# Optimization experiments

Hardware: AMD Instinct MI355X
Metric: run time of the kernel (lower is better)

Reference implementation:

```python
import jax, jax.numpy as jnp
import numpy as np

B, T, C, H = 2, 2048, 1024, 16
HD = C // H          # head_dim = 64
RD = HD // 2         # rotary half-dim = 32


def _rope_tables(T, rd, base=10000.0):
    inv_freq = 1.0 / (base ** (np.arange(rd, dtype=np.float32) / rd))
    t = np.arange(T, dtype=np.float32)
    ang = np.outer(t, inv_freq)  # [T, rd]
    cos = np.cos(ang)[None, :, None, :]  # [1,T,1,rd]
    sin = np.sin(ang)[None, :, None, :]
    return jnp.asarray(cos), jnp.asarray(sin)


def setup_inputs() -> dict:
    key = jax.random.key(0)
    k1, k2, k3 = jax.random.split(key, 3)
    cos, sin = _rope_tables(T, RD)
    return {
        "x": jax.random.normal(k1, (B, T, C), dtype=jnp.float32),
        "cos": cos,
        "sin": sin,
        "W_qkv": jax.random.normal(k2, (C, C), dtype=jnp.float32) / np.sqrt(C),
        "W_proj": jax.random.normal(k3, (C, C), dtype=jnp.float32) / np.sqrt(C),
        "window_left": 512,
    }


def _apply_rotary(x, cos, sin):
    # x: [B,T,H,HD]
    x1, x2 = x[..., :RD], x[..., RD:]
    y1 = x1 * cos + x2 * sin
    y2 = -x1 * sin + x2 * cos
    return jnp.concatenate([y1, y2], axis=-1)


def _rms_norm(x):
    eps = jnp.finfo(x.dtype).eps
    ms = jnp.mean(jnp.square(x), axis=-1, keepdims=True)
    return x * jax.lax.rsqrt(ms + eps)


def reference(x, cos, sin, W_qkv, W_proj, window_left):
    Bx, Tx, Cx = x.shape
    scale = HD ** -0.5
    # tied QKV projection (single matmul)
    w = jnp.einsum("btc,cd->btd", x, W_qkv).reshape(Bx, Tx, H, HD)
    w = _apply_rotary(w, cos, sin)
    w = _rms_norm(w)                      # [B,T,H,HD]
    wq = jnp.transpose(w, (0, 2, 1, 3))    # [B,H,T,HD]
    dots = jnp.einsum("bhqd,bhkd->bhqk", wq, wq) * scale  # [B,H,T,T]
    # causal + sliding-window mask: allow 0 <= (q - k) <= window_left
    i = jnp.arange(Tx)[:, None]
    j = jnp.arange(Tx)[None, :]
    dist = i - j
    allowed = (dist >= 0) & ((window_left <= 0) | (dist <= window_left))
    dots = jnp.where(allowed, dots, -jnp.inf)
    attn = jax.nn.softmax(dots, axis=-1)
    out = jnp.einsum("bhqk,bhkd->bhqd", attn, wq)
    out = jnp.transpose(out, (0, 2, 1, 3)).reshape(Bx, Tx, Cx)
    return jnp.einsum("btc,cd->btd", out, W_proj)
```

## Files before the change

kernel.cpp:

```cpp
#include <hip/hip_runtime.h>
#include <hip/hip_bf16.h>

typedef __bf16 bf16_t;
typedef __bf16 bf16x4 __attribute__((ext_vector_type(4)));
typedef __bf16 bf16x8 __attribute__((ext_vector_type(8)));
typedef float f32x4 __attribute__((ext_vector_type(4)));

#define B_ 2
#define T_ 2048
#define C_ 1024
#define H_ 16
#define HD_ 64
#define RD_ 32
#define M_ (B_ * T_)

__global__ __launch_bounds__(256) void k_prep(const float* __restrict__ x,
                                              bf16_t* __restrict__ xb,
                                              const float* __restrict__ Wq,
                                              bf16_t* __restrict__ wqt,
                                              const float* __restrict__ Wp,
                                              bf16_t* __restrict__ wpt) {
    const int bid = blockIdx.x;
    if (bid < 4096) {
        int i = bid * 256 + threadIdx.x;
        float4 v = reinterpret_cast<const float4*>(x)[i];
        bf16x4 o;
        o[0] = (bf16_t)v.x; o[1] = (bf16_t)v.y; o[2] = (bf16_t)v.z; o[3] = (bf16_t)v.w;
        reinterpret_cast<bf16x4*>(xb)[i] = o;
    } else {
        __shared__ float tile[32][33];
        int b2 = bid - 4096;
        const float* W = (b2 < 1024) ? Wq : Wp;
        bf16_t* Wt = (b2 < 1024) ? wqt : wpt;
        b2 &= 1023;
        const int n0 = (b2 & 31) * 32, k0 = (b2 >> 5) * 32;
        const int tx = threadIdx.x & 31, ty = threadIdx.x >> 5;
        for (int i = ty; i < 32; i += 8)
            tile[i][tx] = W[(size_t)(k0 + i) * C_ + n0 + tx];
        __syncthreads();
        for (int i = ty; i < 32; i += 8)
            Wt[(size_t)(n0 + i) * C_ + k0 + tx] = (bf16_t)tile[tx][i];
    }
}

template <bool FUSED>
__global__ __launch_bounds__(256) void k_gemm(const bf16_t* __restrict__ A,
                                              const bf16_t* __restrict__ Bt,
                                              float* __restrict__ C,
                                              const float* __restrict__ ct,
                                              const float* __restrict__ st,
                                              bf16_t* __restrict__ q,
                                              bf16_t* __restrict__ qT,
                                              int M, int N, int K) {
    constexpr int SMEM_BYTES = FUSED ? 52224 : 49152;
    __shared__ __align__(16) char smem[SMEM_BYTES];
    bf16_t* As = (bf16_t*)smem;
    bf16_t* Bs = (bf16_t*)(smem + 32768);
    const int tid = threadIdx.x;
    const int lane = tid & 63, w = tid >> 6;
    const int wr = w >> 1, wc = w & 1;
    const int g = lane >> 4, li = lane & 15;
    const int bid = blockIdx.x;
    const int work = (bid & 7) * 64 + (bid >> 3);
    const int bx = work & 15;
    const int by = work >> 4;
    const size_t rowA0 = (size_t)by * 128;
    const size_t colB0 = (size_t)bx * 64;
    const bf16_t* Ab = A + rowA0 * K;
    const bf16_t* Bb = Bt + colB0 * K;
    f32x4 acc[4][2] = {};

    const int lr = lane >> 3;
    const int swc = ((lane & 7) ^ lr) * 8;

    auto stage = [&](int buf, int k0) {
        bf16_t* Ad = As + buf * 8192 + (w * 8) * 64;
        bf16_t* Bd = Bs + buf * 4096 + (w * 8) * 64;
#pragma unroll
        for (int a = 0; a < 4; ++a) {
            const bf16_t* src = Ab + (size_t)(a * 32 + w * 8 + lr) * K + k0 + swc;
            __builtin_amdgcn_global_load_lds(
                (const __attribute__((address_space(1))) void*)src,
                (__attribute__((address_space(3))) void*)(Ad + a * 32 * 64), 16, 0, 0);
        }
#pragma unroll
        for (int bq = 0; bq < 2; ++bq) {
            const bf16_t* src = Bb + (size_t)(bq * 32 + w * 8 + lr) * K + k0 + swc;
            __builtin_amdgcn_global_load_lds(
                (const __attribute__((address_space(1))) void*)src,
                (__attribute__((address_space(3))) void*)(Bd + bq * 32 * 64), 16, 0, 0);
        }
    };

    stage(0, 0);
    __syncthreads();
    int cur = 0;
    const int NT = K >> 6;
    for (int kt = 0; kt < NT; ++kt) {
        if (kt < NT - 1) stage(cur ^ 1, (kt + 1) << 6);
        bf16x8 af[4][2], bfr[2][2];
#pragma unroll
        for (int i = 0; i < 4; ++i) {
            const int row = wr * 64 + i * 16 + li;
#pragma unroll
            for (int kk = 0; kk < 2; ++kk)
                af[i][kk] = *(const bf16x8*)(As + cur * 8192 + row * 64 +
                                             (((kk * 4 + g) ^ (li & 7)) * 8));
        }
#pragma unroll
        for (int j = 0; j < 2; ++j) {
            const int row = wc * 32 + j * 16 + li;
#pragma unroll
            for (int kk = 0; kk < 2; ++kk)
                bfr[j][kk] = *(const bf16x8*)(Bs + cur * 4096 + row * 64 +
                                              (((kk * 4 + g) ^ (li & 7)) * 8));
        }
#pragma unroll
        for (int i = 0; i < 4; ++i)
#pragma unroll
            for (int j = 0; j < 2; ++j)
#pragma unroll
                for (int kk = 0; kk < 2; ++kk)
                    acc[i][j] = __builtin_amdgcn_mfma_f32_16x16x32_bf16(
                        af[i][kk], bfr[j][kk], acc[i][j], 0, 0, 0);
        __syncthreads();
        cur ^= 1;
    }

    if constexpr (!FUSED) {
#pragma unroll
        for (int i = 0; i < 4; ++i)
#pragma unroll
            for (int j = 0; j < 2; ++j)
#pragma unroll
                for (int r = 0; r < 4; ++r) {
                    size_t row = rowA0 + wr * 64 + i * 16 + g * 4 + r;
                    size_t col = colB0 + wc * 32 + j * 16 + li;
                    C[row * N + col] = acc[i][j][r];
                }
    } else {
        float* ot = (float*)smem;
        bf16_t* qs = (bf16_t*)(smem + 34816);
#pragma unroll
        for (int i = 0; i < 4; ++i)
#pragma unroll
            for (int j = 0; j < 2; ++j)
#pragma unroll
                for (int r = 0; r < 4; ++r)
                    ot[(wr * 64 + i * 16 + g * 4 + r) * 68 + wc * 32 + j * 16 + li] =
                        acc[i][j][r];
        __syncthreads();
        {
            const int row = tid >> 1, half = tid & 1;
            const int gr = (int)rowA0 + row;
            const int bb = gr >> 11, t = gr & 2047;
            const float* own = ot + row * 68 + half * 32;
            const float* par = ot + row * 68 + (half ^ 1) * 32;
            const float* cp = ct + (size_t)t * RD_;
            const float* sp = st + (size_t)t * RD_;
            float y[32];
            float sq = 0.f;
#pragma unroll
            for (int c4 = 0; c4 < 8; ++c4) {
                float4 xo = ((const float4*)own)[c4];
                float4 xp = ((const float4*)par)[c4];
                float4 cc = ((const float4*)cp)[c4];
                float4 ss = ((const float4*)sp)[c4];
                float* yy = y + c4 * 4;
                if (half == 0) {
                    yy[0] = xo.x * cc.x + xp.x * ss.x;
                    yy[1] = xo.y * cc.y + xp.y * ss.y;
                    yy[2] = xo.z * cc.z + xp.z * ss.z;
                    yy[3] = xo.w * cc.w + xp.w * ss.w;
                } else {
                    yy[0] = xo.x * cc.x - xp.x * ss.x;
                    yy[1] = xo.y * cc.y - xp.y * ss.y;
                    yy[2] = xo.z * cc.z - xp.z * ss.z;
                    yy[3] = xo.w * cc.w - xp.w * ss.w;
                }
                sq += yy[0] * yy[0] + yy[1] * yy[1] + yy[2] * yy[2] + yy[3] * yy[3];
            }
            sq += __shfl_xor(sq, 1);
            const float rn = rsqrtf(sq * (1.0f / 64.0f) + 1.1920929e-7f);
            bf16_t yb[32];
#pragma unroll
            for (int e = 0; e < 32; ++e) yb[e] = (bf16_t)(y[e] * rn);
            bf16_t* qrow = q + (((size_t)bb * H_ + bx) * T_ + t) * 64 + half * 32;
#pragma unroll
            for (int c8 = 0; c8 < 4; ++c8)
                ((bf16x8*)qrow)[c8] = *(const bf16x8*)(yb + c8 * 8);
#pragma unroll
            for (int e = 0; e < 32; ++e)
                qs[(half * 32 + e) * 136 + row] = yb[e];
        }
        __syncthreads();
        {
            const int d = tid >> 2, tq = tid & 3;
            const int bb = (int)(rowA0 >> 11);
            const int t0 = (int)(rowA0 & 2047);
            const bf16_t* srcq = qs + d * 136 + tq * 32;
            bf16_t* dst = qT + (((size_t)bb * H_ + bx) * 64 + d) * T_ + t0 + tq * 32;
#pragma unroll
            for (int c8 = 0; c8 < 4; ++c8)
                ((bf16x8*)dst)[c8] = ((const bf16x8*)srcq)[c8];
        }
    }
}

__global__ __launch_bounds__(256, 4) void k_attn(const bf16_t* __restrict__ q,
                                                 const bf16_t* __restrict__ qT,
                                                 bf16_t* __restrict__ aout,
                                                 const int* __restrict__ wlp) {
    __shared__ bf16_t Ks[2][64][64];
    __shared__ bf16_t Vs[2][64][64];
    __shared__ bf16_t pb[4][16][40];
    const int tid = threadIdx.x;
    const int lane = tid & 63, w = tid >> 6;
    const int g = lane >> 4, li = lane & 15;
    const int bid = blockIdx.x;
    const int work = (bid & 7) * 128 + (bid >> 3);
    const int tb = work & 31;
    const int h = (work >> 5) & 15;
    const int b = work >> 9;
    const int Q0 = tb * 64;
    const bf16_t* base  = q  + ((size_t)(b * H_ + h) * T_) * 64;
    const bf16_t* baseT = qT + ((size_t)(b * H_ + h) * 64) * T_;
    const int wl = wlp[0];
    const int wle = (wl <= 0 || wl > T_) ? T_ : wl;
    const int qw = Q0 + w * 16;
    const int qg = qw + li;

    const int srow = w * 8 + (lane >> 3);
    const int swz = ((lane & 7) ^ (lane >> 3)) * 8;

    bf16x8 aq[2];
    aq[0] = *reinterpret_cast<const bf16x8*>(base + (size_t)(qw + li) * 64 + g * 8);
    aq[1] = *reinterpret_cast<const bf16x8*>(base + (size_t)(qw + li) * 64 + 32 + g * 8);

    f32x4 o[4] = {};
    float m = -1e30f, l = 0.f;
    const float SC = 0.125f * 1.44269504089f;

    const int kb0 = (Q0 > wle) ? ((Q0 - wle) >> 6) : 0;
    const int kb1 = Q0 >> 6;

    auto stageKV = [&](int buf, int J) {
        const bf16_t* ks0 = base + (size_t)(J + srow) * 64 + swz;
        const bf16_t* ks1 = base + (size_t)(J + srow + 32) * 64 + swz;
        const bf16_t* vs0 = baseT + (size_t)srow * T_ + J + swz;
        const bf16_t* vs1 = baseT + (size_t)(srow + 32) * T_ + J + swz;
        __builtin_amdgcn_global_load_lds(
            (const __attribute__((address_space(1))) void*)ks0,
            (__attribute__((address_space(3))) void*)(&Ks[buf][w * 8][0]), 16, 0, 0);
        __builtin_amdgcn_global_load_lds(
            (const __attribute__((address_space(1))) void*)ks1,
            (__attribute__((address_space(3))) void*)(&Ks[buf][w * 8 + 32][0]), 16, 0, 0);
        __builtin_amdgcn_global_load_lds(
            (const __attribute__((address_space(1))) void*)vs0,
            (__attribute__((address_space(3))) void*)(&Vs[buf][w * 8][0]), 16, 0, 0);
        __builtin_amdgcn_global_load_lds(
            (const __attribute__((address_space(1))) void*)vs1,
            (__attribute__((address_space(3))) void*)(&Vs[buf][w * 8 + 32][0]), 16, 0, 0);
    };

    stageKV(0, kb0 << 6);
    __syncthreads();

    int cur = 0;
    for (int kb = kb0; kb <= kb1; ++kb) {
        const int J0 = kb << 6;
        if (kb < kb1) stageKV(cur ^ 1, J0 + 64);
        f32x4 s4[4] = {};
        __builtin_amdgcn_s_setprio(1);
#pragma unroll
        for (int ks = 0; ks < 2; ++ks)
#pragma unroll
            for (int nb = 0; nb < 4; ++nb) {
                const int jl = nb * 16 + li;
                bf16x8 kf = *reinterpret_cast<const bf16x8*>(
                    &Ks[cur][jl][((ks * 4 + g) ^ (jl & 7)) * 8]);
                s4[nb] = __builtin_amdgcn_mfma_f32_16x16x32_bf16(kf, aq[ks], s4[nb], 0, 0, 0);
            }
        __builtin_amdgcn_s_setprio(0);
        float sv[4][4];
        float mn = m;
#pragma unroll
        for (int nb = 0; nb < 4; ++nb)
#pragma unroll
            for (int r = 0; r < 4; ++r) {
                const int j = J0 + nb * 16 + g * 4 + r;
                const int dist = qg - j;
                float x = s4[nb][r] * SC;
                sv[nb][r] = (dist >= 0 && dist <= wle) ? x : -__builtin_inff();
                mn = fmaxf(mn, sv[nb][r]);
            }
        mn = fmaxf(mn, __shfl_xor(mn, 16));
        mn = fmaxf(mn, __shfl_xor(mn, 32));
        const float al = exp2f(m - mn);
        m = mn;
        float la = 0.f;
#pragma unroll
        for (int nb = 0; nb < 4; ++nb)
#pragma unroll
            for (int r = 0; r < 4; ++r) {
                float pv = exp2f(sv[nb][r] - m);
                sv[nb][r] = pv;
                la += pv;
            }
        la += __shfl_xor(la, 16);
        la += __shfl_xor(la, 32);
        l = l * al + la;
        float alq[4];
#pragma unroll
        for (int r = 0; r < 4; ++r) alq[r] = __shfl(al, g * 4 + r);
#pragma unroll
        for (int dnb = 0; dnb < 4; ++dnb)
#pragma unroll
            for (int r = 0; r < 4; ++r) o[dnb][r] *= alq[r];
#pragma unroll
        for (int ks = 0; ks < 2; ++ks) {
#pragma unroll
            for (int nb2 = 0; nb2 < 2; ++nb2) {
                const int nb = ks * 2 + nb2;
                bf16x4 pk;
                pk[0] = (bf16_t)sv[nb][0]; pk[1] = (bf16_t)sv[nb][1];
                pk[2] = (bf16_t)sv[nb][2]; pk[3] = (bf16_t)sv[nb][3];
                *reinterpret_cast<bf16x4*>(&pb[w][li][nb2 * 16 + g * 4]) = pk;
            }
            bf16x8 pa = *reinterpret_cast<const bf16x8*>(&pb[w][li][g * 8]);
            __builtin_amdgcn_s_setprio(1);
#pragma unroll
            for (int dnb = 0; dnb < 4; ++dnb) {
                const int dl = dnb * 16 + li;
                bf16x8 vf = *reinterpret_cast<const bf16x8*>(
                    &Vs[cur][dl][((ks * 4 + g) ^ (dl & 7)) * 8]);
                o[dnb] = __builtin_amdgcn_mfma_f32_16x16x32_bf16(pa, vf, o[dnb], 0, 0, 0);
            }
            __builtin_amdgcn_s_setprio(0);
        }
        __syncthreads();
        cur ^= 1;
    }

    const float rli = 1.0f / l;
    float rlq[4];
#pragma unroll
    for (int r = 0; r < 4; ++r) rlq[r] = __shfl(rli, g * 4 + r);
#pragma unroll
    for (int dnb = 0; dnb < 4; ++dnb)
#pragma unroll
        for (int r = 0; r < 4; ++r) {
            size_t t = (size_t)qw + g * 4 + r;
            aout[((size_t)b * T_ + t) * C_ + h * 64 + dnb * 16 + li] =
                (bf16_t)(o[dnb][r] * rlq[r]);
        }
}

extern "C" void kernel_launch(void* const* d_in, const int* in_sizes, int n_in,
                              void* d_out, int out_size, void* d_ws, size_t ws_size,
                              hipStream_t stream) {
    const float* x     = (const float*)d_in[0];
    const float* ct    = (const float*)d_in[1];
    const float* st    = (const float*)d_in[2];
    const float* Wqkv  = (const float*)d_in[3];
    const float* Wproj = (const float*)d_in[4];
    const int*   wl    = (const int*)d_in[5];
    float* out = (float*)d_out;
    char* ws = (char*)d_ws;

    bf16_t* xb    = (bf16_t*)(ws);
    bf16_t* wqkvt = (bf16_t*)(ws + (8ull << 20));
    bf16_t* wprot = (bf16_t*)(ws + (10ull << 20));
    bf16_t* q     = (bf16_t*)(ws + (12ull << 20));
    bf16_t* qT    = (bf16_t*)(ws + (20ull << 20));
    bf16_t* ao    = (bf16_t*)(ws + (28ull << 20));

    k_prep<<<dim3(6144), dim3(256), 0, stream>>>(x, xb, Wqkv, wqkvt, Wproj, wprot);
    k_gemm<true><<<dim3(512), dim3(256), 0, stream>>>(xb, wqkvt, nullptr, ct, st,
                                                      q, qT, M_, C_, C_);
    k_attn<<<dim3(1024), dim3(256), 0, stream>>>(q, qT, ao, wl);
    k_gemm<false><<<dim3(512), dim3(256), 0, stream>>>(ao, wprot, out, nullptr, nullptr,
                                                       nullptr, nullptr, M_, C_, C_);
}
```

Baseline: 76.21 us.

## Pre-pack Q/V into MFMA fragment layout and load K/V directly from global

The fused QKV GEMM epilogue now writes the normalized Q/K and its transpose in layouts already arranged as MFMA fragments, with 16-row tiles and 64x64 V tiles packed so that each lane's 16-byte chunk sits contiguously. The attention kernel drops the LDS K/V double buffer, async global-to-LDS staging and the per-block syncthreads, and loads fragments straight from global/L2 into registers. Each wave also computes its own key-block range, so it can skip blocks that lie entirely outside its window. This removes LDS traffic and barriers but gives up sharing loaded K/V across the four waves, and global load latency is no longer explicitly overlapped with compute.

```diff
diff --git a/kernel.cpp b/kernel.cpp
--- a/kernel.cpp
+++ b/kernel.cpp
@@ -49,8 +49,8 @@
                                               float* __restrict__ C,
                                               const float* __restrict__ ct,
                                               const float* __restrict__ st,
-                                              bf16_t* __restrict__ q,
-                                              bf16_t* __restrict__ qT,
+                                              bf16_t* __restrict__ qp,
+                                              bf16_t* __restrict__ vp,
                                               int M, int N, int K) {
     constexpr int SMEM_BYTES = FUSED ? 52224 : 49152;
     __shared__ __align__(16) char smem[SMEM_BYTES];
@@ -150,10 +150,10 @@
                     ot[(wr * 64 + i * 16 + g * 4 + r) * 68 + wc * 32 + j * 16 + li] =
                         acc[i][j][r];
         __syncthreads();
+        const int bb = (int)(rowA0 >> 11);
         {
             const int row = tid >> 1, half = tid & 1;
-            const int gr = (int)rowA0 + row;
-            const int bb = gr >> 11, t = gr & 2047;
+            const int t = ((int)rowA0 + row) & 2047;
             const float* own = ot + row * 68 + half * 32;
             const float* par = ot + row * 68 + (half ^ 1) * 32;
             const float* cp = ct + (size_t)t * RD_;
@@ -185,34 +185,37 @@
             bf16_t yb[32];
 #pragma unroll
             for (int e = 0; e < 32; ++e) yb[e] = (bf16_t)(y[e] * rn);
-            bf16_t* qrow = q + (((size_t)bb * H_ + bx) * T_ + t) * 64 + half * 32;
-#pragma unroll
-            for (int c8 = 0; c8 < 4; ++c8)
-                ((bf16x8*)qrow)[c8] = *(const bf16x8*)(yb + c8 * 8);
+            bf16_t* qpb = qp + ((size_t)(bb * H_ + bx) * 128 + (t >> 4)) * 1024;
+#pragma unroll
+            for (int c8 = 0; c8 < 4; ++c8) {
+                const int chunk = (half * 4 + c8) * 16 + (t & 15);
+                *(bf16x8*)(qpb + chunk * 8) = *(const bf16x8*)(yb + c8 * 8);
+            }
 #pragma unroll
             for (int e = 0; e < 32; ++e)
                 qs[(half * 32 + e) * 136 + row] = yb[e];
         }
         __syncthreads();
         {
-            const int d = tid >> 2, tq = tid & 3;
-            const int bb = (int)(rowA0 >> 11);
-            const int t0 = (int)(rowA0 & 2047);
-            const bf16_t* srcq = qs + d * 136 + tq * 32;
-            bf16_t* dst = qT + (((size_t)bb * H_ + bx) * 64 + d) * T_ + t0 + tq * 32;
-#pragma unroll
-            for (int c8 = 0; c8 < 4; ++c8)
-                ((bf16x8*)dst)[c8] = ((const bf16x8*)srcq)[c8];
+            const int d = tid >> 2, jc4 = tid & 3;
+            const int tt0 = (int)((rowA0 & 2047) >> 6);
+            bf16_t* vpb = vp + ((size_t)(bb * H_ + bx) * 32) * 4096;
+#pragma unroll
+            for (int c = 0; c < 4; ++c) {
+                const int jc = jc4 * 4 + c;
+                bf16x8 v8 = *(const bf16x8*)(qs + d * 136 + jc * 8);
+                bf16_t* dst = vpb + (size_t)(tt0 + (jc >> 3)) * 4096 +
+                              ((d >> 4) * 8 + (jc & 7)) * 128 + (d & 15) * 8;
+                *(bf16x8*)dst = v8;
+            }
         }
     }
 }
 
-__global__ __launch_bounds__(256, 4) void k_attn(const bf16_t* __restrict__ q,
-                                                 const bf16_t* __restrict__ qT,
+__global__ __launch_bounds__(256, 4) void k_attn(const bf16_t* __restrict__ qp,
+                                                 const bf16_t* __restrict__ vp,
                                                  bf16_t* __restrict__ aout,
                                                  const int* __restrict__ wlp) {
-    __shared__ bf16_t Ks[2][64][64];
-    __shared__ bf16_t Vs[2][64][64];
     __shared__ bf16_t pb[4][16][40];
     const int tid = threadIdx.x;
     const int lane = tid & 63, w = tid >> 6;
@@ -223,65 +226,52 @@
     const int h = (work >> 5) & 15;
     const int b = work >> 9;
     const int Q0 = tb * 64;
-    const bf16_t* base  = q  + ((size_t)(b * H_ + h) * T_) * 64;
-    const bf16_t* baseT = qT + ((size_t)(b * H_ + h) * 64) * T_;
+    const bf16_t* bq = qp + (size_t)(b * H_ + h) * 131072;
+    const bf16_t* bv = vp + (size_t)(b * H_ + h) * 131072;
     const int wl = wlp[0];
     const int wle = (wl <= 0 || wl > T_) ? T_ : wl;
     const int qw = Q0 + w * 16;
     const int qg = qw + li;
 
-    const int srow = w * 8 + (lane >> 3);
-    const int swz = ((lane & 7) ^ (lane >> 3)) * 8;
+    const int fo = (g * 16 + li) * 8;
+    const int vo = g * 128 + li * 8;
 
     bf16x8 aq[2];
-    aq[0] = *reinterpret_cast<const bf16x8*>(base + (size_t)(qw + li) * 64 + g * 8);
-    aq[1] = *reinterpret_cast<const bf16x8*>(base + (size_t)(qw + li) * 64 + 32 + g * 8);
+    aq[0] = *(const bf16x8*)(bq + (size_t)(qw >> 4) * 1024 + fo);
+    aq[1] = *(const bf16x8*)(bq + (size_t)(qw >> 4) * 1024 + fo + 512);
 
     f32x4 o[4] = {};
     float m = -1e30f, l = 0.f;
     const float SC = 0.125f * 1.44269504089f;
 
-    const int kb0 = (Q0 > wle) ? ((Q0 - wle) >> 6) : 0;
-    const int kb1 = Q0 >> 6;
-
-    auto stageKV = [&](int buf, int J) {
-        const bf16_t* ks0 = base + (size_t)(J + srow) * 64 + swz;
-        const bf16_t* ks1 = base + (size_t)(J + srow + 32) * 64 + swz;
-        const bf16_t* vs0 = baseT + (size_t)srow * T_ + J + swz;
-        const bf16_t* vs1 = baseT + (size_t)(srow + 32) * T_ + J + swz;
-        __builtin_amdgcn_global_load_lds(
-            (const __attribute__((address_space(1))) void*)ks0,
-            (__attribute__((address_space(3))) void*)(&Ks[buf][w * 8][0]), 16, 0, 0);
-        __builtin_amdgcn_global_load_lds(
-            (const __attribute__((address_space(1))) void*)ks1,
-            (__attribute__((address_space(3))) void*)(&Ks[buf][w * 8 + 32][0]), 16, 0, 0);
-        __builtin_amdgcn_global_load_lds(
-            (const __attribute__((address_space(1))) void*)vs0,
-            (__attribute__((address_space(3))) void*)(&Vs[buf][w * 8][0]), 16, 0, 0);
-        __builtin_amdgcn_global_load_lds(
-            (const __attribute__((address_space(1))) void*)vs1,
-            (__attribute__((address_space(3))) void*)(&Vs[buf][w * 8 + 32][0]), 16, 0, 0);
-    };
-
-    stageKV(0, kb0 << 6);
-    __syncthreads();
-
-    int cur = 0;
+    const int kb0 = (qw > wle) ? ((qw - wle) >> 6) : 0;
+    const int kb1 = qw >> 6;
+
     for (int kb = kb0; kb <= kb1; ++kb) {
         const int J0 = kb << 6;
-        if (kb < kb1) stageKV(cur ^ 1, J0 + 64);
+        const bf16_t* kt = bq + (size_t)kb * 4096;
+        const bf16_t* vt = bv + (size_t)kb * 4096;
+        bf16x8 kf[2][4];
+#pragma unroll
+        for (int ks = 0; ks < 2; ++ks)
+#pragma unroll
+            for (int nb = 0; nb < 4; ++nb)
+                kf[ks][nb] = *(const bf16x8*)(kt + nb * 1024 + ks * 512 + fo);
         f32x4 s4[4] = {};
         __builtin_amdgcn_s_setprio(1);
 #pragma unroll
         for (int ks = 0; ks < 2; ++ks)
 #pragma unroll
-            for (int nb = 0; nb < 4; ++nb) {
-                const int jl = nb * 16 + li;
-                bf16x8 kf = *reinterpret_cast<const bf16x8*>(
-                    &Ks[cur][jl][((ks * 4 + g) ^ (jl & 7)) * 8]);
-                s4[nb] = __builtin_amdgcn_mfma_f32_16x16x32_bf16(kf, aq[ks], s4[nb], 0, 0, 0);
-            }
+            for (int nb = 0; nb < 4; ++nb)
+                s4[nb] = __builtin_amdgcn_mfma_f32_16x16x32_bf16(kf[ks][nb], aq[ks],
+                                                                 s4[nb], 0, 0, 0);
         __builtin_amdgcn_s_setprio(0);
+        bf16x8 vf[2][4];
+#pragma unroll
+        for (int ks = 0; ks < 2; ++ks)
+#pragma unroll
+            for (int dnb = 0; dnb < 4; ++dnb)
+                vf[ks][dnb] = *(const bf16x8*)(vt + dnb * 1024 + ks * 512 + vo);
         float sv[4][4];
         float mn = m;
 #pragma unroll
@@ -330,16 +320,11 @@
             bf16x8 pa = *reinterpret_cast<const bf16x8*>(&pb[w][li][g * 8]);
             __builtin_amdgcn_s_setprio(1);
 #pragma unroll
-            for (int dnb = 0; dnb < 4; ++dnb) {
-                const int dl = dnb * 16 + li;
-                bf16x8 vf = *reinterpret_cast<const bf16x8*>(
-                    &Vs[cur][dl][((ks * 4 + g) ^ (dl & 7)) * 8]);
-                o[dnb] = __builtin_amdgcn_mfma_f32_16x16x32_bf16(pa, vf, o[dnb], 0, 0, 0);
-            }
+            for (int dnb = 0; dnb < 4; ++dnb)
+                o[dnb] = __builtin_amdgcn_mfma_f32_16x16x32_bf16(pa, vf[ks][dnb],
+                                                                 o[dnb], 0, 0, 0);
             __builtin_amdgcn_s_setprio(0);
         }
-        __syncthreads();
-        cur ^= 1;
     }
 
     const float rli = 1.0f / l;
@@ -371,14 +356,14 @@
     bf16_t* xb    = (bf16_t*)(ws);
     bf16_t* wqkvt = (bf16_t*)(ws + (8ull << 20));
     bf16_t* wprot = (bf16_t*)(ws + (10ull << 20));
-    bf16_t* q     = (bf16_t*)(ws + (12ull << 20));
-    bf16_t* qT    = (bf16_t*)(ws + (20ull << 20));
+    bf16_t* qp    = (bf16_t*)(ws + (12ull << 20));
+    bf16_t* vp    = (bf16_t*)(ws + (20ull << 20));
     bf16_t* ao    = (bf16_t*)(ws + (28ull << 20));
 
     k_prep<<<dim3(6144), dim3(256), 0, stream>>>(x, xb, Wqkv, wqkvt, Wproj, wprot);
     k_gemm<true><<<dim3(512), dim3(256), 0, stream>>>(xb, wqkvt, nullptr, ct, st,
-                                                      q, qT, M_, C_, C_);
-    k_attn<<<dim3(1024), dim3(256), 0, stream>>>(q, qT, ao, wl);
+                                                      qp, vp, M_, C_, C_);
+    k_attn<<<dim3(1024), dim3(256), 0, stream>>>(qp, vp, ao, wl);
     k_gemm<false><<<dim3(512), dim3(256), 0, stream>>>(ao, wprot, out, nullptr, nullptr,
                                                        nullptr, nullptr, M_, C_, C_);
 }
```

Result: faster. 69.14 us (-9.3%).
